# Kernel tuning notes

Hardware: AMD Instinct MI355X
Metric: run time of the kernel (lower is better)

The kernel has to match this reference:

```python
import jax, jax.numpy as jnp
import numpy as np

B = 2_097_152          # batch of theta samples
POLY_DEG = 127         # QSP polynomial degree -> 128 phases
PI = np.float32(np.pi)


def setup_inputs() -> dict:
    key = jax.random.key(0)
    k1, k2 = jax.random.split(key)
    th = jax.random.uniform(k1, (B, 1), dtype=jnp.float32) * PI
    phis = jax.random.uniform(k2, (POLY_DEG + 1, 1), dtype=jnp.float32) * PI
    return {"th": th, "phis": phis}


def reference(th, phis):
    # th: [B,1] float32, phis: [P+1,1] float32 (learned QSP phases)
    theta = th[:, 0]                      # [B]
    c = jnp.cos(theta)
    s = jnp.sin(theta)
    # expm(i*theta*X) = cos(theta) I + i sin(theta) X  (closed form, no expm)
    wx = jnp.stack(
        [jnp.stack([c + 0j, 1j * s], axis=-1),
         jnp.stack([1j * s, c + 0j], axis=-1)],
        axis=-2,
    ).astype(jnp.complex64)               # [B,2,2]

    phi = phis[:, 0]                      # [P+1]
    e = jnp.exp(1j * phi).astype(jnp.complex64)
    # expm(i*phi*Z) = diag(e^{i phi}, e^{-i phi})
    rz = (jnp.zeros((phi.shape[0], 2, 2), jnp.complex64)
          .at[:, 0, 0].set(e)
          .at[:, 1, 1].set(jnp.conj(e)))  # [P+1,2,2]

    u0 = jnp.broadcast_to(rz[0], (theta.shape[0], 2, 2))  # [B,2,2]

    def step(u, rzk):
        u = jnp.einsum('bij,bjk->bik', u, wx)   # u @ W(x)
        u = jnp.einsum('bij,jk->bik', u, rzk)   # ... @ Rz(phi_k)
        return u, None

    u, _ = jax.lax.scan(step, u0, rz[1:])       # 127 sequential steps
    # convention == 0: (Re[u_00], Im[u_00])
    return (jnp.real(u[:, 0, 0]), jnp.imag(u[:, 0, 0]))
```

## Files before the change

kernel.cpp:

```cpp
#include <hip/hip_runtime.h>


__device__ __forceinline__ float wave_shr1(float x) {
    return __builtin_bit_cast(float,
        __builtin_amdgcn_update_dpp(0, __builtin_bit_cast(int, x),
                                    0x138, 0xf, 0xf, true));
}

__device__ __forceinline__ float rlane(float x, int l) {
    return __builtin_bit_cast(float,
        __builtin_amdgcn_readlane(__builtin_bit_cast(int, x), l));
}

__global__ __launch_bounds__(256, 4) void qsp_fused(
    const float* __restrict__ th,
    const float* __restrict__ phis,
    float* __restrict__ out,
    int Bq8)
{
    const int tid  = threadIdx.x;
    const int lane = tid & 63;
    const int idx  = blockIdx.x * blockDim.x + tid;
    const int lidx = (idx < Bq8) ? idx : 0;

    const float4 ta = ((const float4*)th)[2 * lidx];
    const float4 tb = ((const float4*)th)[2 * lidx + 1];

    float sp, cp;
    __sincosf(phis[lane], &sp, &cp);
    const float hAx = 0.5f * cp, hAy = 0.5f * sp;
    __sincosf(phis[lane + 64], &sp, &cp);
    const float hBx = 0.5f * cp, hBy = 0.5f * sp;

    float A0r = 0.f, A0i = 0.f, B0r = 0.f, B0i = 0.f;
    float A1r = 0.f, A1i = 0.f, B1r = 0.f, B1i = 0.f;
    const float h0x = rlane(hAx, 0), h0y = rlane(hAy, 0);
    if (lane == 0) { A0r = 2.f * h0x; A0i = 2.f * h0y; }

    #define QSP_REC(hx_, hy_)                                                 \
    {                                                                         \
        const float hx = (hx_), hy = (hy_);                                   \
        const float pAr = wave_shr1(A1r), pAi = wave_shr1(A1i);               \
        const float pBr = wave_shr1(B1r), pBi = wave_shr1(B1i);               \
        const float u0r = pAr + pBr, u0i = pAi + pBi;                         \
        const float v0r = A0r - B0r, v0i = A0i - B0i;                         \
        const float sA0r = u0r + v0r, sA0i = u0i + v0i;                       \
        const float sB0r = u0r - v0r, sB0i = u0i - v0i;                       \
        const float u1r = A0r + B0r, u1i = A0i + B0i;                         \
        const float v1r = A1r - B1r, v1i = A1i - B1i;                         \
        const float sA1r = u1r + v1r, sA1i = u1i + v1i;                       \
        const float sB1r = u1r - v1r, sB1i = u1i - v1i;                       \
        A0r = fmaf(hx, sA0r, -hy * sA0i);                                     \
        A0i = fmaf(hx, sA0i,  hy * sA0r);                                     \
        B0r = fmaf(hx, sB0r,  hy * sB0i);                                     \
        B0i = fmaf(hx, sB0i, -hy * sB0r);                                     \
        A1r = fmaf(hx, sA1r, -hy * sA1i);                                     \
        A1i = fmaf(hx, sA1i,  hy * sA1r);                                     \
        B1r = fmaf(hx, sB1r,  hy * sB1i);                                     \
        B1i = fmaf(hx, sB1i, -hy * sB1r);                                     \
    }

    #pragma unroll 4
    for (int k = 1; k < 64; ++k)   QSP_REC(rlane(hAx, k), rlane(hAy, k))
    #pragma unroll 4
    for (int k = 0; k < 64; ++k)   QSP_REC(rlane(hBx, k), rlane(hBy, k))
    #undef QSP_REC

    const float th8[8] = {ta.x, ta.y, ta.z, ta.w, tb.x, tb.y, tb.z, tb.w};
    float zr[8], zi[8];
    #pragma unroll
    for (int e = 0; e < 8; ++e) {
        float s, c;
        __sincosf(2.f * th8[e], &s, &c);
        zr[e] = c; zi[e] = s;
    }

    float ar[8], ai[8];
    #pragma unroll
    for (int e = 0; e < 8; ++e) { ar[e] = 0.f; ai[e] = 0.f; }

    #define QSP_STEP(gr, gi)                                                  \
        _Pragma("unroll")                                                     \
        for (int e = 0; e < 8; ++e) {                                         \
            const float nr = fmaf(ar[e], zr[e], fmaf(-ai[e], zi[e], (gr)));   \
            const float ni = fmaf(ar[e], zi[e], fmaf( ai[e], zr[e], (gi)));   \
            ar[e] = nr; ai[e] = ni;                                           \
        }

    #pragma unroll 2
    for (int jj = 63; jj >= 0; --jj) {
        const float g1r = rlane(A1r, jj), g1i = rlane(A1i, jj);
        QSP_STEP(g1r, g1i)
        const float g0r = rlane(A0r, jj), g0i = rlane(A0i, jj);
        QSP_STEP(g0r, g0i)
    }
    #undef QSP_STEP

    float orv[8], oiv[8];
    #pragma unroll
    for (int e = 0; e < 8; ++e) {
        float S, C;
        __sincosf(127.f * th8[e], &S, &C);
        orv[e] = fmaf(ar[e], C,  ai[e] * S);
        oiv[e] = fmaf(ai[e], C, -ar[e] * S);
    }

    if (idx < Bq8) {
        float4* o4 = (float4*)out;
        const int ib = 2 * Bq8;
        o4[2 * idx]          = make_float4(orv[0], orv[1], orv[2], orv[3]);
        o4[2 * idx + 1]      = make_float4(orv[4], orv[5], orv[6], orv[7]);
        o4[ib + 2 * idx]     = make_float4(oiv[0], oiv[1], oiv[2], oiv[3]);
        o4[ib + 2 * idx + 1] = make_float4(oiv[4], oiv[5], oiv[6], oiv[7]);
    }
}

extern "C" void kernel_launch(void* const* d_in, const int* in_sizes, int n_in,
                              void* d_out, int out_size, void* d_ws, size_t ws_size,
                              hipStream_t stream)
{
    const float* th   = (const float*)d_in[0];
    const float* phis = (const float*)d_in[1];
    float* out = (float*)d_out;
    const int B = in_sizes[0];
    const int Bq8 = B >> 3;
    const int block = 256;
    const int grid = (Bq8 + block - 1) / block;
    qsp_fused<<<grid, block, 0, stream>>>(th, phis, out, Bq8);
}
```

Baseline: 103.1 us.

## Compute QSP coefficients in one wave per block and use packed FMA Horner

```diff
diff --git a/kernel.cpp b/kernel.cpp
--- a/kernel.cpp
+++ b/kernel.cpp
@@ -1,5 +1,7 @@
 #include <hip/hip_runtime.h>
 
+
+typedef __attribute__((ext_vector_type(2))) float f32x2;
 
 __device__ __forceinline__ float wave_shr1(float x) {
     return __builtin_bit_cast(float,
@@ -18,91 +20,105 @@
     float* __restrict__ out,
     int Bq8)
 {
+    __shared__ float4 gsh[64];
+
     const int tid  = threadIdx.x;
     const int lane = tid & 63;
+    const int wv   = tid >> 6;
+    const int gwv  = blockIdx.x & 3;
     const int idx  = blockIdx.x * blockDim.x + tid;
     const int lidx = (idx < Bq8) ? idx : 0;
 
     const float4 ta = ((const float4*)th)[2 * lidx];
     const float4 tb = ((const float4*)th)[2 * lidx + 1];
 
-    float sp, cp;
-    __sincosf(phis[lane], &sp, &cp);
-    const float hAx = 0.5f * cp, hAy = 0.5f * sp;
-    __sincosf(phis[lane + 64], &sp, &cp);
-    const float hBx = 0.5f * cp, hBy = 0.5f * sp;
+    if (wv == gwv) {
+        float sp, cp;
+        __sincosf(phis[lane], &sp, &cp);
+        const float hAx = 0.5f * cp, hAy = 0.5f * sp;
+        __sincosf(phis[lane + 64], &sp, &cp);
+        const float hBx = 0.5f * cp, hBy = 0.5f * sp;
 
-    float A0r = 0.f, A0i = 0.f, B0r = 0.f, B0i = 0.f;
-    float A1r = 0.f, A1i = 0.f, B1r = 0.f, B1i = 0.f;
-    const float h0x = rlane(hAx, 0), h0y = rlane(hAy, 0);
-    if (lane == 0) { A0r = 2.f * h0x; A0i = 2.f * h0y; }
+        float A0r = 0.f, A0i = 0.f, B0r = 0.f, B0i = 0.f;
+        float A1r = 0.f, A1i = 0.f, B1r = 0.f, B1i = 0.f;
+        const float h0x = rlane(hAx, 0), h0y = rlane(hAy, 0);
+        if (lane == 0) { A0r = 2.f * h0x; A0i = 2.f * h0y; }
 
-    #define QSP_REC(hx_, hy_)                                                 \
-    {                                                                         \
-        const float hx = (hx_), hy = (hy_);                                   \
-        const float pAr = wave_shr1(A1r), pAi = wave_shr1(A1i);               \
-        const float pBr = wave_shr1(B1r), pBi = wave_shr1(B1i);               \
-        const float u0r = pAr + pBr, u0i = pAi + pBi;                         \
-        const float v0r = A0r - B0r, v0i = A0i - B0i;                         \
-        const float sA0r = u0r + v0r, sA0i = u0i + v0i;                       \
-        const float sB0r = u0r - v0r, sB0i = u0i - v0i;                       \
-        const float u1r = A0r + B0r, u1i = A0i + B0i;                         \
-        const float v1r = A1r - B1r, v1i = A1i - B1i;                         \
-        const float sA1r = u1r + v1r, sA1i = u1i + v1i;                       \
-        const float sB1r = u1r - v1r, sB1i = u1i - v1i;                       \
-        A0r = fmaf(hx, sA0r, -hy * sA0i);                                     \
-        A0i = fmaf(hx, sA0i,  hy * sA0r);                                     \
-        B0r = fmaf(hx, sB0r,  hy * sB0i);                                     \
-        B0i = fmaf(hx, sB0i, -hy * sB0r);                                     \
-        A1r = fmaf(hx, sA1r, -hy * sA1i);                                     \
-        A1i = fmaf(hx, sA1i,  hy * sA1r);                                     \
-        B1r = fmaf(hx, sB1r,  hy * sB1i);                                     \
-        B1i = fmaf(hx, sB1i, -hy * sB1r);                                     \
+        #define QSP_REC(hx_, hy_)                                             \
+        {                                                                     \
+            const float hx = (hx_), hy = (hy_);                               \
+            const float pAr = wave_shr1(A1r), pAi = wave_shr1(A1i);           \
+            const float pBr = wave_shr1(B1r), pBi = wave_shr1(B1i);           \
+            const float u0r = pAr + pBr, u0i = pAi + pBi;                     \
+            const float v0r = A0r - B0r, v0i = A0i - B0i;                     \
+            const float sA0r = u0r + v0r, sA0i = u0i + v0i;                   \
+            const float sB0r = u0r - v0r, sB0i = u0i - v0i;                   \
+            const float u1r = A0r + B0r, u1i = A0i + B0i;                     \
+            const float v1r = A1r - B1r, v1i = A1i - B1i;                     \
+            const float sA1r = u1r + v1r, sA1i = u1i + v1i;                   \
+            const float sB1r = u1r - v1r, sB1i = u1i - v1i;                   \
+            A0r = fmaf(hx, sA0r, -hy * sA0i);                                 \
+            A0i = fmaf(hx, sA0i,  hy * sA0r);                                 \
+            B0r = fmaf(hx, sB0r,  hy * sB0i);                                 \
+            B0i = fmaf(hx, sB0i, -hy * sB0r);                                 \
+            A1r = fmaf(hx, sA1r, -hy * sA1i);                                 \
+            A1i = fmaf(hx, sA1i,  hy * sA1r);                                 \
+            B1r = fmaf(hx, sB1r,  hy * sB1i);                                 \
+            B1i = fmaf(hx, sB1i, -hy * sB1r);                                 \
+        }
+        #pragma unroll 4
+        for (int k = 1; k < 64; ++k)   QSP_REC(rlane(hAx, k), rlane(hAy, k))
+        #pragma unroll 4
+        for (int k = 0; k < 64; ++k)   QSP_REC(rlane(hBx, k), rlane(hBy, k))
+        #undef QSP_REC
+
+        gsh[lane] = make_float4(A0r, A0i, A1r, A1i);
     }
 
-    #pragma unroll 4
-    for (int k = 1; k < 64; ++k)   QSP_REC(rlane(hAx, k), rlane(hAy, k))
-    #pragma unroll 4
-    for (int k = 0; k < 64; ++k)   QSP_REC(rlane(hBx, k), rlane(hBy, k))
-    #undef QSP_REC
-
     const float th8[8] = {ta.x, ta.y, ta.z, ta.w, tb.x, tb.y, tb.z, tb.w};
-    float zr[8], zi[8];
+    f32x2 Z[8], W2[8], ACC[8];
     #pragma unroll
     for (int e = 0; e < 8; ++e) {
         float s, c;
         __sincosf(2.f * th8[e], &s, &c);
-        zr[e] = c; zi[e] = s;
+        Z[e]  = (f32x2){c, s};
+        W2[e] = (f32x2){-s, c};
+        ACC[e] = (f32x2){0.f, 0.f};
     }
 
-    float ar[8], ai[8];
-    #pragma unroll
-    for (int e = 0; e < 8; ++e) { ar[e] = 0.f; ai[e] = 0.f; }
+    __syncthreads();
 
-    #define QSP_STEP(gr, gi)                                                  \
+    const float4 g = gsh[lane];
+    const float G0r = g.x, G0i = g.y, G1r = g.z, G1i = g.w;
+
+    #define QSP_STEP_PK(Gv)                                                   \
         _Pragma("unroll")                                                     \
         for (int e = 0; e < 8; ++e) {                                         \
-            const float nr = fmaf(ar[e], zr[e], fmaf(-ai[e], zi[e], (gr)));   \
-            const float ni = fmaf(ar[e], zi[e], fmaf( ai[e], zr[e], (gi)));   \
-            ar[e] = nr; ai[e] = ni;                                           \
+            f32x2 T, A2;                                                      \
+            asm("v_pk_fma_f32 %0, %1, %2, %3 op_sel:[0,0,0] op_sel_hi:[0,1,1]"\
+                : "=v"(T) : "v"(ACC[e]), "v"(Z[e]), "v"(Gv));                 \
+            asm("v_pk_fma_f32 %0, %1, %2, %3 op_sel:[1,0,0] op_sel_hi:[1,1,1]"\
+                : "=v"(A2) : "v"(ACC[e]), "v"(W2[e]), "v"(T));                \
+            ACC[e] = A2;                                                      \
         }
 
     #pragma unroll 2
     for (int jj = 63; jj >= 0; --jj) {
-        const float g1r = rlane(A1r, jj), g1i = rlane(A1i, jj);
-        QSP_STEP(g1r, g1i)
-        const float g0r = rlane(A0r, jj), g0i = rlane(A0i, jj);
-        QSP_STEP(g0r, g0i)
+        const f32x2 Gt1 = {rlane(G1r, jj), rlane(G1i, jj)};
+        QSP_STEP_PK(Gt1)
+        const f32x2 Gt0 = {rlane(G0r, jj), rlane(G0i, jj)};
+        QSP_STEP_PK(Gt0)
     }
-    #undef QSP_STEP
+    #undef QSP_STEP_PK
 
     float orv[8], oiv[8];
     #pragma unroll
     for (int e = 0; e < 8; ++e) {
         float S, C;
         __sincosf(127.f * th8[e], &S, &C);
-        orv[e] = fmaf(ar[e], C,  ai[e] * S);
-        oiv[e] = fmaf(ai[e], C, -ar[e] * S);
+        const float arv = ACC[e].x, aiv = ACC[e].y;
+        orv[e] = fmaf(arv, C,  aiv * S);
+        oiv[e] = fmaf(aiv, C, -arv * S);
     }
 
     if (idx < Bq8) {
```

Result: faster. 90.51 us (-12.2%).
